# Performance work log

Measured on AMD Instinct MI355X. Metric: run time of the kernel, lower is better.

## Reference

```python
import jax, jax.numpy as jnp
import numpy as np

CAPACITY_FACTOR = 0.5
AUX_LOSS_WEIGHT = 0.01


def setup_inputs() -> dict:
    key = jax.random.key(0)
    ks = jax.random.split(key, 4)
    B, L, D = 4, 4096, 2048
    H = 4 * D
    x = jax.random.normal(ks[0], (B, L, D), dtype=jnp.float32)
    w_router = jax.random.normal(ks[1], (D,), dtype=jnp.float32) * (1.0 / np.sqrt(D))
    W1 = jax.random.normal(ks[2], (D, H), dtype=jnp.float32) * (1.0 / np.sqrt(D))
    b1 = jnp.zeros((H,), dtype=jnp.float32)
    W2 = jax.random.normal(ks[3], (H, D), dtype=jnp.float32) * (1.0 / np.sqrt(H))
    b2 = jnp.zeros((D,), dtype=jnp.float32)
    return {"x": x, "w_router": w_router, "W1": W1, "b1": b1, "W2": W2, "b2": b2}


def _ffn(t, W1, b1, W2, b2):
    # canonical transformer FFN block applied to selected tokens
    return jax.nn.gelu(t @ W1 + b1) @ W2 + b2


def reference(x, w_router, W1, b1, W2, b2):
    B, L, D = x.shape
    capacity = max(1, int(L * CAPACITY_FACTOR))

    # --- MoDRouter (eval mode: no noise) ---
    router_logits = jnp.einsum("bld,d->bl", x, w_router)          # [B, L]
    _, top_idx = jax.lax.top_k(router_logits, capacity)           # [B, capacity]
    router_probs = jax.nn.sigmoid(router_logits)                  # [B, L]
    aux_loss = AUX_LOSS_WEIGHT * jnp.mean(
        (jnp.mean(router_probs, axis=-1) - CAPACITY_FACTOR) ** 2)

    # --- gather selected tokens, run block, scatter back ---
    b_idx = jnp.arange(B)[:, None]                                # [B, 1]
    selected = x[b_idx, top_idx]                                  # [B, capacity, D]
    processed = _ffn(selected, W1, b1, W2, b2)                    # [B, capacity, D]
    output = x.at[b_idx, top_idx].set(processed)                  # [B, L, D]

    # --- sigmoid-blended residual ---
    w = router_probs[..., None]                                   # [B, L, 1]
    final = w * output + (1.0 - w) * x
    return final, aux_loss
```

## Files before the change

kernel.cpp:

```cpp
#include <hip/hip_runtime.h>
#include <stdint.h>

#define NB 4
#define LL 4096
#define DD 2048
#define HH 8192
#define CAP 2048
#define BLD (NB * LL * DD)

typedef __attribute__((ext_vector_type(8))) short bf16x8;
typedef __attribute__((ext_vector_type(4))) float f32x4;
typedef __attribute__((ext_vector_type(8))) unsigned short u16x8;

__device__ __forceinline__ ushort f2b(float f) {
  union { float f; uint32_t u; } c; c.f = f;
  uint32_t u = c.u;
  return (ushort)((u + 0x7FFFu + ((u >> 16) & 1u)) >> 16);
}
__device__ __forceinline__ float b2f(ushort h) {
  union { uint32_t u; float f; } c; c.u = ((uint32_t)h) << 16;
  return c.f;
}

__global__ void init_kernel(float* probsum, int* cnts) {
  int t = threadIdx.x;
  if (t < NB) probsum[t] = 0.f;
  if (t < 2 * NB) cnts[t] = 0;
}

__global__ void __launch_bounds__(256) router_kernel(
    const float* __restrict__ x, const float* __restrict__ wr,
    uint32_t* __restrict__ keys, float* __restrict__ probs,
    float* __restrict__ probsum) {
  int tok = blockIdx.x;
  int t = threadIdx.x;
  const float4* xr = (const float4*)(x + (size_t)tok * DD);
  const float4* wv = (const float4*)wr;
  float4 a0 = xr[2 * t], a1 = xr[2 * t + 1];
  float4 w0 = wv[2 * t], w1 = wv[2 * t + 1];
  float s = a0.x * w0.x + a0.y * w0.y + a0.z * w0.z + a0.w * w0.w +
            a1.x * w1.x + a1.y * w1.y + a1.z * w1.z + a1.w * w1.w;
  for (int o = 32; o; o >>= 1) s += __shfl_down(s, o, 64);
  __shared__ float red[4];
  int wave = t >> 6, lane = t & 63;
  if (lane == 0) red[wave] = s;
  __syncthreads();
  if (t == 0) {
    float logit = red[0] + red[1] + red[2] + red[3];
    float p = 1.f / (1.f + __expf(-logit));
    probs[tok] = p;
    union { float f; uint32_t u; } c; c.f = logit;
    uint32_t u = c.u;
    keys[tok] = (u & 0x80000000u) ? ~u : (u | 0x80000000u);
    atomicAdd(&probsum[tok >> 12], p);
  }
}

__global__ void __launch_bounds__(256) thresh_kernel(
    const uint32_t* __restrict__ keys, uint32_t* __restrict__ Vout,
    int* __restrict__ cgt) {
  int b = blockIdx.x;
  __shared__ uint32_t k_[LL];
  __shared__ int red[4];
  int t = threadIdx.x;
  for (int i = t; i < LL; i += 256) k_[i] = keys[b * LL + i];
  __syncthreads();
  uint32_t cur = 0;
  for (int bit = 31; bit >= 0; --bit) {
    uint32_t cand = cur | (1u << bit);
    int c = 0;
    for (int i = t; i < LL; i += 256) c += (k_[i] >= cand) ? 1 : 0;
    for (int o = 32; o; o >>= 1) c += __shfl_down(c, o, 64);
    if ((t & 63) == 0) red[t >> 6] = c;
    __syncthreads();
    int tot = red[0] + red[1] + red[2] + red[3];
    if (tot >= CAP) cur = cand;
    __syncthreads();
  }
  int c = 0;
  for (int i = t; i < LL; i += 256) c += (k_[i] > cur) ? 1 : 0;
  for (int o = 32; o; o >>= 1) c += __shfl_down(c, o, 64);
  if ((t & 63) == 0) red[t >> 6] = c;
  __syncthreads();
  if (t == 0) {
    Vout[b] = cur;
    cgt[b] = red[0] + red[1] + red[2] + red[3];
  }
}

__global__ void __launch_bounds__(256) select_kernel(
    const uint32_t* __restrict__ keys, const uint32_t* __restrict__ V,
    const int* __restrict__ cgt, int* __restrict__ cnts,
    int* __restrict__ sel_idx, int* __restrict__ tok2slot) {
  int i = blockIdx.x * 256 + threadIdx.x;
  int b = i >> 12, l = i & (LL - 1);
  uint32_t k = keys[i], v = V[b];
  int slot = -1;
  if (k > v) {
    slot = atomicAdd(&cnts[b], 1);
  } else if (k == v) {
    int e = atomicAdd(&cnts[NB + b], 1);
    int s = CAP - 1 - e;
    if (s >= cgt[b]) slot = s;
  }
  tok2slot[i] = slot;
  if (slot >= 0) sel_idx[b * CAP + slot] = l;
}

__global__ void __launch_bounds__(256) gather_kernel(
    const float* __restrict__ x, const int* __restrict__ sel_idx,
    ushort* __restrict__ xsel) {
  int r = blockIdx.x;
  int b = r >> 11, s = r & (CAP - 1);
  int l = sel_idx[b * CAP + s];
  int t = threadIdx.x;
  const float4* src = (const float4*)(x + ((size_t)(b * LL + l)) * DD);
  float4 a0 = src[2 * t], a1 = src[2 * t + 1];
  u16x8 o;
  o[0] = f2b(a0.x); o[1] = f2b(a0.y); o[2] = f2b(a0.z); o[3] = f2b(a0.w);
  o[4] = f2b(a1.x); o[5] = f2b(a1.y); o[6] = f2b(a1.z); o[7] = f2b(a1.w);
  ((u16x8*)(xsel + (size_t)r * DD))[t] = o;
}

__global__ void transpose_kernel(const float* __restrict__ in,
                                 ushort* __restrict__ out, int R, int C) {
  __shared__ float tile[32][33];
  int c0 = blockIdx.x * 32, r0 = blockIdx.y * 32;
  int tx = threadIdx.x, ty = threadIdx.y;
#pragma unroll
  for (int i = 0; i < 4; i++)
    tile[ty + i * 8][tx] = in[(size_t)(r0 + ty + i * 8) * C + c0 + tx];
  __syncthreads();
#pragma unroll
  for (int i = 0; i < 4; i++)
    out[(size_t)(c0 + ty + i * 8) * R + r0 + tx] = f2b(tile[tx][ty + i * 8]);
}

__device__ __forceinline__ void gemm_core(const ushort* __restrict__ A,
                                          const ushort* __restrict__ BT,
                                          int K, int rowA0, int colB0,
                                          ushort* As, ushort* Bs,
                                          f32x4 acc[4][4]) {
  int t = threadIdx.x;
  int wave = t >> 6, lane = t & 63;
  int wr = wave >> 1, wc = wave & 1;
  int lrow = lane & 15;
  int lk = (lane >> 4) << 3;
  int r0 = t >> 2;
  int c0 = (t & 3) << 3;
  const ushort* Ag = A + (size_t)(rowA0 + r0) * K + c0;
  const ushort* Ag2 = Ag + (size_t)64 * K;
  const ushort* Bg = BT + (size_t)(colB0 + r0) * K + c0;
  const ushort* Bg2 = Bg + (size_t)64 * K;
  char* AsB = (char*)As;
  char* BsB = (char*)Bs;
  for (int kt = 0; kt < K; kt += 32) {
    __builtin_amdgcn_global_load_lds(
        (const __attribute__((address_space(1))) void*)(Ag + kt),
        (__attribute__((address_space(3))) void*)(AsB + wave * 1024), 16, 0, 0);
    __builtin_amdgcn_global_load_lds(
        (const __attribute__((address_space(1))) void*)(Ag2 + kt),
        (__attribute__((address_space(3))) void*)(AsB + 4096 + wave * 1024), 16, 0, 0);
    __builtin_amdgcn_global_load_lds(
        (const __attribute__((address_space(1))) void*)(Bg + kt),
        (__attribute__((address_space(3))) void*)(BsB + wave * 1024), 16, 0, 0);
    __builtin_amdgcn_global_load_lds(
        (const __attribute__((address_space(1))) void*)(Bg2 + kt),
        (__attribute__((address_space(3))) void*)(BsB + 4096 + wave * 1024), 16, 0, 0);
    __syncthreads();
    bf16x8 aF[4], bF[4];
    const ushort* Asr = As + (wr * 64 + lrow) * 32 + lk;
    const ushort* Bsr = Bs + (wc * 64 + lrow) * 32 + lk;
#pragma unroll
    for (int m = 0; m < 4; m++) aF[m] = *(const bf16x8*)(Asr + m * 16 * 32);
#pragma unroll
    for (int n = 0; n < 4; n++) bF[n] = *(const bf16x8*)(Bsr + n * 16 * 32);
#pragma unroll
    for (int m = 0; m < 4; m++)
#pragma unroll
      for (int n = 0; n < 4; n++)
        acc[m][n] = __builtin_amdgcn_mfma_f32_16x16x32_bf16(aF[m], bF[n],
                                                            acc[m][n], 0, 0, 0);
    __syncthreads();
  }
}

__global__ void __launch_bounds__(256) gemm1_kernel(
    const ushort* __restrict__ A, const ushort* __restrict__ BT,
    const float* __restrict__ b1, ushort* __restrict__ hOut) {
  __shared__ ushort As[128 * 32], Bs[128 * 32];
  f32x4 acc[4][4];
#pragma unroll
  for (int m = 0; m < 4; m++)
#pragma unroll
    for (int n = 0; n < 4; n++) acc[m][n] = (f32x4){0.f, 0.f, 0.f, 0.f};
  int tm = blockIdx.y * 128, tn = blockIdx.x * 128;
  gemm_core(A, BT, DD, tm, tn, As, Bs, acc);
  int t = threadIdx.x, wave = t >> 6, lane = t & 63;
  int wr = wave >> 1, wc = wave & 1;
  int colBase = tn + wc * 64 + (lane & 15);
  int rowBase = tm + wr * 64 + ((lane >> 4) << 2);
#pragma unroll
  for (int m = 0; m < 4; m++)
#pragma unroll
    for (int n = 0; n < 4; n++) {
      int col = colBase + n * 16;
      float bias = b1[col];
#pragma unroll
      for (int r = 0; r < 4; r++) {
        int row = rowBase + m * 16 + r;
        float v = acc[m][n][r] + bias;
        float u = 1.5957691216057308f * (v + 0.044715f * v * v * v);
        float g = v / (1.f + __expf(-u));
        hOut[(size_t)row * HH + col] = f2b(g);
      }
    }
}

__global__ void __launch_bounds__(256) gemm2_kernel(
    const ushort* __restrict__ A, const ushort* __restrict__ BT,
    const float* __restrict__ b2, ushort* __restrict__ out_sel) {
  __shared__ ushort As[128 * 32], Bs[128 * 32];
  f32x4 acc[4][4];
#pragma unroll
  for (int m = 0; m < 4; m++)
#pragma unroll
    for (int n = 0; n < 4; n++) acc[m][n] = (f32x4){0.f, 0.f, 0.f, 0.f};
  int tm = blockIdx.y * 128, tn = blockIdx.x * 128;
  gemm_core(A, BT, HH, tm, tn, As, Bs, acc);
  int t = threadIdx.x, wave = t >> 6, lane = t & 63;
  int wr = wave >> 1, wc = wave & 1;
  int colBase = tn + wc * 64 + (lane & 15);
  int rowBase = tm + wr * 64 + ((lane >> 4) << 2);
#pragma unroll
  for (int m = 0; m < 4; m++)
#pragma unroll
    for (int n = 0; n < 4; n++) {
      int col = colBase + n * 16;
      float bias = b2[col];
#pragma unroll
      for (int r = 0; r < 4; r++) {
        int row = rowBase + m * 16 + r;
        out_sel[(size_t)row * DD + col] = f2b(acc[m][n][r] + bias);
      }
    }
}

__global__ void __launch_bounds__(256) final_kernel(
    const float* __restrict__ x, const float* __restrict__ probs,
    const int* __restrict__ tok2slot, const ushort* __restrict__ out_sel,
    float* __restrict__ outF) {
  int tok = blockIdx.x;
  int b = tok >> 12;
  int slot = tok2slot[tok];
  float p = probs[tok];
  int t = threadIdx.x;
  const float4* xr = (const float4*)(x + (size_t)tok * DD);
  float4* od = (float4*)(outF + (size_t)tok * DD);
  float4 a0 = xr[2 * t], a1 = xr[2 * t + 1];
  if (slot >= 0) {
    u16x8 q = ((const u16x8*)(out_sel + ((size_t)((b << 11) + slot)) * DD))[t];
    float q1p = 1.f - p;
    a0.x = p * b2f(q[0]) + q1p * a0.x;
    a0.y = p * b2f(q[1]) + q1p * a0.y;
    a0.z = p * b2f(q[2]) + q1p * a0.z;
    a0.w = p * b2f(q[3]) + q1p * a0.w;
    a1.x = p * b2f(q[4]) + q1p * a1.x;
    a1.y = p * b2f(q[5]) + q1p * a1.y;
    a1.z = p * b2f(q[6]) + q1p * a1.z;
    a1.w = p * b2f(q[7]) + q1p * a1.w;
  }
  od[2 * t] = a0;
  od[2 * t + 1] = a1;
}

__global__ void aux_kernel(const float* __restrict__ probsum,
                           float* __restrict__ outaux) {
  if (threadIdx.x == 0) {
    float s = 0.f;
#pragma unroll
    for (int b = 0; b < NB; b++) {
      float m = probsum[b] * (1.f / (float)LL) - 0.5f;
      s += m * m;
    }
    outaux[0] = 0.01f * s * (1.f / (float)NB);
  }
}

extern "C" void kernel_launch(void* const* d_in, const int* in_sizes, int n_in,
                              void* d_out, int out_size, void* d_ws,
                              size_t ws_size, hipStream_t stream) {
  const float* x = (const float*)d_in[0];
  const float* w_router = (const float*)d_in[1];
  const float* W1 = (const float*)d_in[2];
  const float* b1 = (const float*)d_in[3];
  const float* W2 = (const float*)d_in[4];
  const float* b2 = (const float*)d_in[5];
  float* outF = (float*)d_out;

  char* w = (char*)d_ws;
  uint32_t* keys   = (uint32_t*)(w);
  float*    probs  = (float*)(w + 65536);
  float*    probsum= (float*)(w + 131072);
  int*      cnts   = (int*)(w + 131328);
  uint32_t* V      = (uint32_t*)(w + 131584);
  int*      cgt    = (int*)(w + 131840);
  int*      sel_idx= (int*)(w + 132096);
  int*      tok2slot=(int*)(w + 164864);
  ushort*   xsel   = (ushort*)(w + 230400);
  ushort*   W1T    = (ushort*)(w + 230400 + 33554432);
  ushort*   W2T    = (ushort*)(w + 230400 + 2 * 33554432);
  ushort*   out_sel= (ushort*)(w + 230400 + (size_t)3 * 33554432);

  ushort* hbuf = (ushort*)d_out;

  init_kernel<<<1, 64, 0, stream>>>(probsum, cnts);
  router_kernel<<<NB * LL, 256, 0, stream>>>(x, w_router, keys, probs, probsum);
  thresh_kernel<<<NB, 256, 0, stream>>>(keys, V, cgt);
  select_kernel<<<NB * LL / 256, 256, 0, stream>>>(keys, V, cgt, cnts, sel_idx,
                                                   tok2slot);
  gather_kernel<<<NB * CAP, 256, 0, stream>>>(x, sel_idx, xsel);
  transpose_kernel<<<dim3(HH / 32, DD / 32), dim3(32, 8), 0, stream>>>(W1, W1T,
                                                                       DD, HH);
  transpose_kernel<<<dim3(DD / 32, HH / 32), dim3(32, 8), 0, stream>>>(W2, W2T,
                                                                       HH, DD);
  gemm1_kernel<<<dim3(HH / 128, NB * CAP / 128), 256, 0, stream>>>(xsel, W1T,
                                                                   b1, hbuf);
  gemm2_kernel<<<dim3(DD / 128, NB * CAP / 128), 256, 0, stream>>>(hbuf, W2T,
                                                                   b2, out_sel);
  final_kernel<<<NB * LL, 256, 0, stream>>>(x, probs, tok2slot, out_sel, outF);
  aux_kernel<<<1, 64, 0, stream>>>(probsum, outF + BLD);
}
```

Before: 1.399 ms.

## Replace GEMMs with 256x256 double-buffered, swizzled, phase-interleaved MFMA kernel

Both FFN GEMMs move from 128x128 tiles with a single LDS buffer and full syncs onto one templated 256x256-tile kernel with 512 threads. The new kernel double-buffers 64-wide K slices in LDS, splits each K step into four MFMA phases interleaved with async global-to-LDS loads, XOR-swizzles LDS columns to avoid bank conflicts, raises wave priority around MFMA bursts, and remaps workgroups for L2 locality. The aim is to hide memory latency and raise data reuse per tile. In exchange it uses 128KB of LDS per block and hand-placed waitcnt and barrier ordering that is easy to get wrong.

```diff
diff --git a/kernel.cpp b/kernel.cpp
--- a/kernel.cpp
+++ b/kernel.cpp
@@ -136,114 +136,188 @@
     out[(size_t)(c0 + ty + i * 8) * R + r0 + tx] = f2b(tile[tx][ty + i * 8]);
 }
 
-__device__ __forceinline__ void gemm_core(const ushort* __restrict__ A,
-                                          const ushort* __restrict__ BT,
-                                          int K, int rowA0, int colB0,
-                                          ushort* As, ushort* Bs,
-                                          f32x4 acc[4][4]) {
-  int t = threadIdx.x;
-  int wave = t >> 6, lane = t & 63;
-  int wr = wave >> 1, wc = wave & 1;
-  int lrow = lane & 15;
-  int lk = (lane >> 4) << 3;
-  int r0 = t >> 2;
-  int c0 = (t & 3) << 3;
-  const ushort* Ag = A + (size_t)(rowA0 + r0) * K + c0;
-  const ushort* Ag2 = Ag + (size_t)64 * K;
-  const ushort* Bg = BT + (size_t)(colB0 + r0) * K + c0;
-  const ushort* Bg2 = Bg + (size_t)64 * K;
-  char* AsB = (char*)As;
-  char* BsB = (char*)Bs;
-  for (int kt = 0; kt < K; kt += 32) {
-    __builtin_amdgcn_global_load_lds(
-        (const __attribute__((address_space(1))) void*)(Ag + kt),
-        (__attribute__((address_space(3))) void*)(AsB + wave * 1024), 16, 0, 0);
-    __builtin_amdgcn_global_load_lds(
-        (const __attribute__((address_space(1))) void*)(Ag2 + kt),
-        (__attribute__((address_space(3))) void*)(AsB + 4096 + wave * 1024), 16, 0, 0);
-    __builtin_amdgcn_global_load_lds(
-        (const __attribute__((address_space(1))) void*)(Bg + kt),
-        (__attribute__((address_space(3))) void*)(BsB + wave * 1024), 16, 0, 0);
-    __builtin_amdgcn_global_load_lds(
-        (const __attribute__((address_space(1))) void*)(Bg2 + kt),
-        (__attribute__((address_space(3))) void*)(BsB + 4096 + wave * 1024), 16, 0, 0);
-    __syncthreads();
-    bf16x8 aF[4], bF[4];
-    const ushort* Asr = As + (wr * 64 + lrow) * 32 + lk;
-    const ushort* Bsr = Bs + (wc * 64 + lrow) * 32 + lk;
-#pragma unroll
-    for (int m = 0; m < 4; m++) aF[m] = *(const bf16x8*)(Asr + m * 16 * 32);
-#pragma unroll
-    for (int n = 0; n < 4; n++) bF[n] = *(const bf16x8*)(Bsr + n * 16 * 32);
+#define MFMA_(d, a, b) d = __builtin_amdgcn_mfma_f32_16x16x32_bf16(a, b, d, 0, 0, 0)
+
+template <int K, int N, bool GELU>
+__global__ __launch_bounds__(512, 2) void gemm256_kernel(
+    const ushort* __restrict__ A, const ushort* __restrict__ BT,
+    const float* __restrict__ bias, ushort* __restrict__ C) {
+  __shared__ char lds[131072];
+  char* ldsC = (char*)lds;
+  const int t = threadIdx.x;
+  const int wave = t >> 6, lane = t & 63;
+  const int wr = wave >> 2, wc = wave & 3;
+
+  int gx = gridDim.x;
+  int nwg = gx * gridDim.y;
+  int flat = blockIdx.y * gx + blockIdx.x;
+  int swzb = (flat & 7) * (nwg >> 3) + (flat >> 3);
+  int bm = (swzb / gx) * 256;
+  int bn = (swzb % gx) * 256;
+
+  const int rr = t >> 3;
+  const int scb = ((t & 7) << 4) ^ (((t >> 5) & 1) << 5);
+  const size_t j1off = (size_t)64 * K * 2;
+  const char* srcA0 = (const char*)A + ((size_t)(bm + rr) * K) * 2 + scb;
+  const char* srcA1 = (const char*)A + ((size_t)(bm + 128 + rr) * K) * 2 + scb;
+  const char* srcB0 = (const char*)BT + ((size_t)(bn + rr) * K) * 2 + scb;
+  const char* srcB1 = (const char*)BT + ((size_t)(bn + 128 + rr) * K) * 2 + scb;
+
+#define STAGE(srcPtr, kb, ldsOff)                                                   \
+  do {                                                                              \
+    __builtin_amdgcn_global_load_lds(                                               \
+        (const __attribute__((address_space(1))) void*)((srcPtr) + (kb)),           \
+        (__attribute__((address_space(3))) void*)(ldsC + (ldsOff) + wave * 1024),   \
+        16, 0, 0);                                                                  \
+    __builtin_amdgcn_global_load_lds(                                               \
+        (const __attribute__((address_space(1))) void*)((srcPtr) + (kb) + j1off),   \
+        (__attribute__((address_space(3))) void*)(ldsC + (ldsOff) + 8192 + wave * 1024), \
+        16, 0, 0);                                                                  \
+  } while (0)
+
+  const int l15 = lane & 15;
+  const int g = lane >> 4;
+  const int swzr = ((lane >> 2) & 1) << 5;
+  const int cb0 = (g << 4) ^ swzr;
+  const int cb1 = (64 | (g << 4)) ^ swzr;
+  const int rb = l15 << 7;
+
+  f32x4 acc[8][4];
+#pragma unroll
+  for (int m = 0; m < 8; m++)
+#pragma unroll
+    for (int n = 0; n < 4; n++) acc[m][n] = (f32x4){0.f, 0.f, 0.f, 0.f};
+
+  bf16x8 alo[4][2], ahi[4][2], b01[2][2], b23[2][2];
+  const int NT = K / 64;
+
+  STAGE(srcA0, 0, 0);
+  STAGE(srcA1, 0, 16384);
+  STAGE(srcB0, 0, 32768);
+  STAGE(srcB1, 0, 49152);
+  STAGE(srcA0, 128, 65536 + 0);
+  STAGE(srcA1, 128, 65536 + 16384);
+  asm volatile("s_waitcnt vmcnt(4)" ::: "memory");
+  __builtin_amdgcn_sched_barrier(0);
+  __builtin_amdgcn_s_barrier();
+
+  for (int kt = 0; kt < NT; ++kt) {
+    const int p = kt & 1;
+    const int bufP = p << 16, bufQ = (p ^ 1) << 16;
+    const char* aP = ldsC + bufP + wr * 16384 + rb;
+    const char* bP = ldsC + bufP + 32768 + ((wc >> 1) * 16384) + ((wc & 1) * 8192) + rb;
+    const size_t kb1 = (size_t)(kt + 1) << 7;
+    const size_t kb2 = (size_t)(kt + 2) << 7;
+
+#pragma unroll
+    for (int m = 0; m < 4; m++) {
+      alo[m][0] = *(const bf16x8*)(aP + (m << 11) + cb0);
+      alo[m][1] = *(const bf16x8*)(aP + (m << 11) + cb1);
+    }
+#pragma unroll
+    for (int n = 0; n < 2; n++) {
+      b01[n][0] = *(const bf16x8*)(bP + (n << 11) + cb0);
+      b01[n][1] = *(const bf16x8*)(bP + (n << 11) + cb1);
+    }
+    if (kt + 1 < NT) STAGE(srcB0, kb1, bufQ + 32768);
+    __builtin_amdgcn_s_barrier();
+    asm volatile("s_waitcnt lgkmcnt(0)" ::: "memory");
+    __builtin_amdgcn_sched_barrier(0);
+    __builtin_amdgcn_s_setprio(1);
 #pragma unroll
     for (int m = 0; m < 4; m++)
 #pragma unroll
-      for (int n = 0; n < 4; n++)
-        acc[m][n] = __builtin_amdgcn_mfma_f32_16x16x32_bf16(aF[m], bF[n],
-                                                            acc[m][n], 0, 0, 0);
-    __syncthreads();
-  }
-}
-
-__global__ void __launch_bounds__(256) gemm1_kernel(
-    const ushort* __restrict__ A, const ushort* __restrict__ BT,
-    const float* __restrict__ b1, ushort* __restrict__ hOut) {
-  __shared__ ushort As[128 * 32], Bs[128 * 32];
-  f32x4 acc[4][4];
-#pragma unroll
-  for (int m = 0; m < 4; m++)
-#pragma unroll
-    for (int n = 0; n < 4; n++) acc[m][n] = (f32x4){0.f, 0.f, 0.f, 0.f};
-  int tm = blockIdx.y * 128, tn = blockIdx.x * 128;
-  gemm_core(A, BT, DD, tm, tn, As, Bs, acc);
-  int t = threadIdx.x, wave = t >> 6, lane = t & 63;
-  int wr = wave >> 1, wc = wave & 1;
-  int colBase = tn + wc * 64 + (lane & 15);
-  int rowBase = tm + wr * 64 + ((lane >> 4) << 2);
-#pragma unroll
-  for (int m = 0; m < 4; m++)
+      for (int n = 0; n < 2; n++) {
+        MFMA_(acc[m][n], alo[m][0], b01[n][0]);
+        MFMA_(acc[m][n], alo[m][1], b01[n][1]);
+      }
+    __builtin_amdgcn_s_setprio(0);
+    __builtin_amdgcn_s_barrier();
+
+#pragma unroll
+    for (int m = 0; m < 4; m++) {
+      ahi[m][0] = *(const bf16x8*)(aP + ((m + 4) << 11) + cb0);
+      ahi[m][1] = *(const bf16x8*)(aP + ((m + 4) << 11) + cb1);
+    }
+    if (kt + 1 < NT) STAGE(srcB1, kb1, bufQ + 49152);
+    __builtin_amdgcn_s_barrier();
+    asm volatile("s_waitcnt lgkmcnt(0)" ::: "memory");
+    __builtin_amdgcn_sched_barrier(0);
+    __builtin_amdgcn_s_setprio(1);
+#pragma unroll
+    for (int m = 0; m < 4; m++)
+#pragma unroll
+      for (int n = 0; n < 2; n++) {
+        MFMA_(acc[m + 4][n], ahi[m][0], b01[n][0]);
+        MFMA_(acc[m + 4][n], ahi[m][1], b01[n][1]);
+      }
+    __builtin_amdgcn_s_setprio(0);
+    __builtin_amdgcn_s_barrier();
+
+#pragma unroll
+    for (int n = 0; n < 2; n++) {
+      b23[n][0] = *(const bf16x8*)(bP + ((n + 2) << 11) + cb0);
+      b23[n][1] = *(const bf16x8*)(bP + ((n + 2) << 11) + cb1);
+    }
+    if (kt + 2 < NT) STAGE(srcA0, kb2, bufP + 0);
+    __builtin_amdgcn_s_barrier();
+    asm volatile("s_waitcnt lgkmcnt(0)" ::: "memory");
+    __builtin_amdgcn_sched_barrier(0);
+    __builtin_amdgcn_s_setprio(1);
+#pragma unroll
+    for (int m = 0; m < 4; m++)
+#pragma unroll
+      for (int n = 0; n < 2; n++) {
+        MFMA_(acc[m + 4][n + 2], ahi[m][0], b23[n][0]);
+        MFMA_(acc[m + 4][n + 2], ahi[m][1], b23[n][1]);
+      }
+    __builtin_amdgcn_s_setprio(0);
+    __builtin_amdgcn_s_barrier();
+
+    if (kt + 2 < NT) STAGE(srcA1, kb2, bufP + 16384);
+    __builtin_amdgcn_s_barrier();
+    __builtin_amdgcn_s_setprio(1);
+#pragma unroll
+    for (int m = 0; m < 4; m++)
+#pragma unroll
+      for (int n = 0; n < 2; n++) {
+        MFMA_(acc[m][n + 2], alo[m][0], b23[n][0]);
+        MFMA_(acc[m][n + 2], alo[m][1], b23[n][1]);
+      }
+    __builtin_amdgcn_s_setprio(0);
+    if (kt + 1 < NT) {
+      if (kt + 2 < NT) {
+        asm volatile("s_waitcnt vmcnt(4)" ::: "memory");
+      } else {
+        asm volatile("s_waitcnt vmcnt(0)" ::: "memory");
+      }
+      __builtin_amdgcn_sched_barrier(0);
+    }
+    __builtin_amdgcn_s_barrier();
+  }
+
+  const int colBase = bn + wc * 64 + l15;
+  const int rowBase = bm + wr * 128 + (g << 2);
+  float bs[4];
+#pragma unroll
+  for (int n = 0; n < 4; n++) bs[n] = bias[colBase + n * 16];
+#pragma unroll
+  for (int m = 0; m < 8; m++)
 #pragma unroll
     for (int n = 0; n < 4; n++) {
       int col = colBase + n * 16;
-      float bias = b1[col];
 #pragma unroll
       for (int r = 0; r < 4; r++) {
         int row = rowBase + m * 16 + r;
-        float v = acc[m][n][r] + bias;
-        float u = 1.5957691216057308f * (v + 0.044715f * v * v * v);
-        float g = v / (1.f + __expf(-u));
-        hOut[(size_t)row * HH + col] = f2b(g);
-      }
-    }
-}
-
-__global__ void __launch_bounds__(256) gemm2_kernel(
-    const ushort* __restrict__ A, const ushort* __restrict__ BT,
-    const float* __restrict__ b2, ushort* __restrict__ out_sel) {
-  __shared__ ushort As[128 * 32], Bs[128 * 32];
-  f32x4 acc[4][4];
-#pragma unroll
-  for (int m = 0; m < 4; m++)
-#pragma unroll
-    for (int n = 0; n < 4; n++) acc[m][n] = (f32x4){0.f, 0.f, 0.f, 0.f};
-  int tm = blockIdx.y * 128, tn = blockIdx.x * 128;
-  gemm_core(A, BT, HH, tm, tn, As, Bs, acc);
-  int t = threadIdx.x, wave = t >> 6, lane = t & 63;
-  int wr = wave >> 1, wc = wave & 1;
-  int colBase = tn + wc * 64 + (lane & 15);
-  int rowBase = tm + wr * 64 + ((lane >> 4) << 2);
-#pragma unroll
-  for (int m = 0; m < 4; m++)
-#pragma unroll
-    for (int n = 0; n < 4; n++) {
-      int col = colBase + n * 16;
-      float bias = b2[col];
-#pragma unroll
-      for (int r = 0; r < 4; r++) {
-        int row = rowBase + m * 16 + r;
-        out_sel[(size_t)row * DD + col] = f2b(acc[m][n][r] + bias);
-      }
-    }
+        float v = acc[m][n][r] + bs[n];
+        if (GELU) {
+          float u = 1.5957691216057308f * (v + 0.044715f * v * v * v);
+          v = v / (1.f + __expf(-u));
+        }
+        C[(size_t)row * N + col] = f2b(v);
+      }
+    }
+#undef STAGE
 }
 
 __global__ void __launch_bounds__(256) final_kernel(
@@ -299,18 +373,18 @@
   float* outF = (float*)d_out;
 
   char* w = (char*)d_ws;
-  uint32_t* keys   = (uint32_t*)(w);
-  float*    probs  = (float*)(w + 65536);
-  float*    probsum= (float*)(w + 131072);
-  int*      cnts   = (int*)(w + 131328);
-  uint32_t* V      = (uint32_t*)(w + 131584);
-  int*      cgt    = (int*)(w + 131840);
-  int*      sel_idx= (int*)(w + 132096);
-  int*      tok2slot=(int*)(w + 164864);
-  ushort*   xsel   = (ushort*)(w + 230400);
-  ushort*   W1T    = (ushort*)(w + 230400 + 33554432);
-  ushort*   W2T    = (ushort*)(w + 230400 + 2 * 33554432);
-  ushort*   out_sel= (ushort*)(w + 230400 + (size_t)3 * 33554432);
+  uint32_t* keys    = (uint32_t*)(w);
+  float*    probs   = (float*)(w + 65536);
+  float*    probsum = (float*)(w + 131072);
+  int*      cnts    = (int*)(w + 131328);
+  uint32_t* V       = (uint32_t*)(w + 131584);
+  int*      cgt     = (int*)(w + 131840);
+  int*      sel_idx = (int*)(w + 132096);
+  int*      tok2slot= (int*)(w + 164864);
+  ushort*   xsel    = (ushort*)(w + 230400);
+  ushort*   W1T     = (ushort*)(w + 230400 + 33554432);
+  ushort*   W2T     = (ushort*)(w + 230400 + 2 * 33554432);
+  ushort*   out_sel = (ushort*)(w + 230400 + (size_t)3 * 33554432);
 
   ushort* hbuf = (ushort*)d_out;
 
@@ -324,10 +398,10 @@
                                                                        DD, HH);
   transpose_kernel<<<dim3(DD / 32, HH / 32), dim3(32, 8), 0, stream>>>(W2, W2T,
                                                                        HH, DD);
-  gemm1_kernel<<<dim3(HH / 128, NB * CAP / 128), 256, 0, stream>>>(xsel, W1T,
-                                                                   b1, hbuf);
-  gemm2_kernel<<<dim3(DD / 128, NB * CAP / 128), 256, 0, stream>>>(hbuf, W2T,
-                                                                   b2, out_sel);
+  gemm256_kernel<DD, HH, true>
+      <<<dim3(HH / 256, (NB * CAP) / 256), 512, 0, stream>>>(xsel, W1T, b1, hbuf);
+  gemm256_kernel<HH, DD, false>
+      <<<dim3(DD / 256, (NB * CAP) / 256), 512, 0, stream>>>(hbuf, W2T, b2, out_sel);
   final_kernel<<<NB * LL, 256, 0, stream>>>(x, probs, tok2slot, out_sel, outF);
   aux_kernel<<<1, 64, 0, stream>>>(probsum, outF + BLD);
 }
```

New measurement: 1.177 ms. -15.9%, faster.
